# Performance work log

Hardware: AMD Instinct MI355X
Metric: run time of the kernel (lower is better)

Reference implementation:

```python
import jax, jax.numpy as jnp
import numpy as np

H = 256          # hidden_size
K = 3            # pointer hops
LAMDA = 3.0
EPS = 1e-8       # torch cosine_similarity eps
# dropout is treated as eval-mode (identity)


def _gru_cell(x, h, wi, wh, bi, bh):
    # torch GRUCell: gate order reset, update, new
    gx = x @ wi.T + bi            # (B, 3*4H)
    gh = h @ wh.T + bh
    xr, xz, xn = jnp.split(gx, 3, axis=-1)
    hr, hz, hn = jnp.split(gh, 3, axis=-1)
    r = jax.nn.sigmoid(xr + hr)
    z = jax.nn.sigmoid(xz + hz)
    n = jnp.tanh(xn + r * hn)
    return (1.0 - z) * n + z * h


def setup_inputs() -> dict:
    key = jax.random.key(0)
    ks = jax.random.split(key, 16)
    B, L = 128, 512
    d2, d4 = 2 * H, 4 * H
    sc = lambda i, shape, fan: jax.random.normal(ks[i], shape, jnp.float32) * (1.0 / np.sqrt(fan))
    return {
        "m": jax.random.normal(ks[0], (B, L, d2), jnp.float32),
        "s1": jax.random.normal(ks[1], (B, d4), jnp.float32),
        "s2": jax.random.normal(ks[2], (B, d4), jnp.float32),
        "s3": jax.random.normal(ks[3], (B, d4), jnp.float32),
        "m_mask": jnp.ones((B, L), jnp.int32),
        "w2_w": sc(4, (d2, d2), d2), "w2_b": jnp.zeros((d2,), jnp.float32),
        "w3_w": sc(5, (d4, d2), d4), "w3_b": jnp.zeros((d2,), jnp.float32),
        "w4_w": sc(6, (d4, d4), d4), "w4_b": jnp.zeros((d4,), jnp.float32),
        "w5_w": sc(7, (d4, 1), d4), "w5_b": jnp.zeros((1,), jnp.float32),
        "gru_wi": sc(8, (3 * d4, d2), d2),
        "gru_wh": sc(9, (3 * d4, d4), d4),
        "gru_bi": jnp.zeros((3 * d4,), jnp.float32),
        "gru_bh": jnp.zeros((3 * d4,), jnp.float32),
    }


def reference(m, s1, s2, s3, m_mask,
              w2_w, w2_b, w3_w, w3_b, w4_w, w4_b, w5_w, w5_b,
              gru_wi, gru_wh, gru_bi, gru_bh):
    # m: (B, L, 2H); s*: (B, 4H); m_mask: (B, L)
    mtt = m @ w2_w + w2_b                         # (B, L, 2H), loop-invariant
    m_norm = jnp.maximum(jnp.linalg.norm(mtt, axis=-1), EPS)  # (B, L)
    invalid = m_mask == 0

    def branch(st):
        for _ in range(K):
            stt = st @ w3_w + w3_b                # (B, 2H)
            s_norm = jnp.maximum(jnp.linalg.norm(stt, axis=-1), EPS)  # (B,)
            dot = jnp.einsum('bld,bd->bl', mtt, stt)
            att = LAMDA * dot / (m_norm * s_norm[:, None])
            att = jnp.where(invalid, -jnp.inf, att)
            p = jax.nn.softmax(att, axis=1)       # (B, L)
            f_att = jnp.einsum('bl,bld->bd', p, m)  # (B, 2H)
            st = _gru_cell(f_att, st, gru_wi, gru_wh, gru_bi, gru_bh)
        h = jax.nn.relu(st @ w4_w + w4_b)         # (B, 4H)
        return (h @ w5_w + w5_b)[:, 0]            # (B,)

    result = jnp.stack([branch(s1), branch(s2), branch(s3)], axis=1)  # (B, 3)
    return jax.nn.log_softmax(result, axis=1)
```

## Files before the change

kernel.cpp:

```cpp
#include <hip/hip_runtime.h>
#include <math.h>

constexpr int B  = 128;
constexpr int L  = 512;
constexpr int D2 = 512;
constexpr int D4 = 1024;
constexpr int G3 = 3072;
constexpr int R3 = 384;
constexpr int NC = 4096;
constexpr float LAMDA = 3.0f;
constexpr float EPSF  = 1e-8f;

typedef __attribute__((ext_vector_type(8))) short bf16x8;
typedef __attribute__((ext_vector_type(8))) short short8;
typedef __attribute__((ext_vector_type(4))) float f32x4;

__device__ __forceinline__ ushort f2bf(float v) {
  uint u = __builtin_bit_cast(uint, v);
  u = (u + 0x7fffu + ((u >> 16) & 1u)) >> 16;
  return (ushort)u;
}
__device__ __forceinline__ float bf2f(ushort h) {
  return __builtin_bit_cast(float, (uint)h << 16);
}
__device__ __forceinline__ float bflo(uint w) { return __builtin_bit_cast(float, w << 16); }
__device__ __forceinline__ float bfhi(uint w) { return __builtin_bit_cast(float, w & 0xffff0000u); }
__device__ __forceinline__ void split2(float v, ushort& h, ushort& l) {
  h = f2bf(v);
  l = f2bf(v - bf2f(h));
}
__device__ __forceinline__ void gload_lds16(const void* g, void* l) {
  __builtin_amdgcn_global_load_lds(
      (const __attribute__((address_space(1))) unsigned int*)g,
      (__attribute__((address_space(3))) unsigned int*)l, 16, 0, 0);
}

__global__ void k_init(const float* __restrict__ s1, const float* __restrict__ s2,
                       const float* __restrict__ s3, float* __restrict__ st3,
                       ushort* __restrict__ sth, ushort* __restrict__ stl,
                       float* __restrict__ snacc, float* __restrict__ cacc,
                       float* __restrict__ o3) {
  int idx = blockIdx.x * blockDim.x + threadIdx.x;
  if (idx < R3) { snacc[idx] = 0.f; cacc[idx] = 0.f; o3[idx] = 0.f; }
  int total = R3 * D4;
  for (; idx < total; idx += gridDim.x * blockDim.x) {
    int r = idx / D4, i = idx - r * D4;
    int k = r / B, b = r - k * B;
    const float* s = (k == 0) ? s1 : (k == 1) ? s2 : s3;
    float v = s[b * D4 + i];
    st3[idx] = v;
    if (sth) { ushort h, l; split2(v, h, l); sth[idx] = h; stl[idx] = l; }
  }
}

__global__ void k_conv_m(const float* __restrict__ m, ushort* __restrict__ mbf) {
  int idx = blockIdx.x * blockDim.x + threadIdx.x;
  const int total8 = (B * L * D2) / 8;
  for (; idx < total8; idx += gridDim.x * blockDim.x) {
    const float4* p = reinterpret_cast<const float4*>(m) + (size_t)idx * 2;
    float4 a = p[0], c = p[1];
    ushort o[8] = {f2bf(a.x), f2bf(a.y), f2bf(a.z), f2bf(a.w),
                   f2bf(c.x), f2bf(c.y), f2bf(c.z), f2bf(c.w)};
    *reinterpret_cast<uint4*>(mbf + (size_t)idx * 8) = *reinterpret_cast<const uint4*>(o);
  }
}

__global__ void k_w2t(const float* __restrict__ w2, ushort* __restrict__ w2t) {
  __shared__ ushort t[64][65];
  int bk = (blockIdx.x & 7) * 64, bn = (blockIdx.x >> 3) * 64;
  int tid = threadIdx.x;
#pragma unroll
  for (int i = 0; i < 16; ++i) {
    int e = tid + i * 256; int r = e >> 6, c = e & 63;
    t[r][c] = f2bf(w2[(bk + r) * 512 + bn + c]);
  }
  __syncthreads();
#pragma unroll
  for (int i = 0; i < 16; ++i) {
    int e = tid + i * 256; int r = e >> 6, c = e & 63;
    w2t[(bn + r) * 512 + bk + c] = t[c][r];
  }
}

__global__ void k_split_direct(const float* __restrict__ in, ushort* __restrict__ oh,
                               ushort* __restrict__ ol, int n4) {
  int idx = blockIdx.x * blockDim.x + threadIdx.x;
  for (; idx < n4; idx += gridDim.x * blockDim.x) {
    float4 v = reinterpret_cast<const float4*>(in)[idx];
    ushort4 h, l;
    split2(v.x, h.x, l.x); split2(v.y, h.y, l.y);
    split2(v.z, h.z, l.z); split2(v.w, h.w, l.w);
    reinterpret_cast<ushort4*>(oh)[idx] = h;
    reinterpret_cast<ushort4*>(ol)[idx] = l;
  }
}

__global__ void k_split_trans(const float* __restrict__ in, int K, int N,
                              ushort* __restrict__ oh, ushort* __restrict__ ol) {
  __shared__ float t[64][65];
  int bk = blockIdx.x * 64, bn = blockIdx.y * 64;
  int tid = threadIdx.x;
#pragma unroll
  for (int i = 0; i < 16; ++i) {
    int e = tid + i * 256; int r = e >> 6, c = e & 63;
    t[r][c] = in[(size_t)(bk + r) * N + bn + c];
  }
  __syncthreads();
#pragma unroll
  for (int i = 0; i < 16; ++i) {
    int e = tid + i * 256; int r = e >> 6, c = e & 63;
    ushort h, l;
    split2(t[c][r], h, l);
    oh[(size_t)(bn + r) * K + bk + c] = h;
    ol[(size_t)(bn + r) * K + bk + c] = l;
  }
}

__global__ void k_bcat2(const float* __restrict__ w3b, const float* __restrict__ gbh,
                        const float* __restrict__ w2w, float* __restrict__ bcat) {
  int idx = blockIdx.x * 256 + threadIdx.x;
  if (idx < D2) bcat[idx] = w3b[idx];
  else if (idx < D2 + G3) bcat[idx] = gbh[idx - D2];
  else if (idx < NC) {
    int e = idx - (D2 + G3);
    float s = 0.f;
    for (int d = 0; d < D2; ++d) s = fmaf(w3b[d], w2w[(size_t)e * D2 + d], s);
    bcat[idx] = s;
  }
}

__global__ __launch_bounds__(64) void k_gemm_wf(
    const ushort* __restrict__ Ahp, const ushort* __restrict__ Alp,
    const ushort* __restrict__ Bhp, const ushort* __restrict__ Blp,
    ushort* __restrict__ Ch, ushort* __restrict__ Cl) {
  const int ln = threadIdx.x;
  const int lrow = ln & 15, lk = ln >> 4;
  const int rowb = blockIdx.y * 64;
  const int colb = blockIdx.x * 64;
  size_t aoff[4], boff[4];
#pragma unroll
  for (int f = 0; f < 4; ++f) {
    aoff[f] = (size_t)(rowb + f * 16 + lrow) * D2 + lk * 8;
    boff[f] = (size_t)(colb + f * 16 + lrow) * D2 + lk * 8;
  }
  f32x4 acc[4][4] = {};
  for (int kc = 0; kc < D2; kc += 32) {
    bf16x8 ah[4], al[4], bh[4], bl[4];
#pragma unroll
    for (int f = 0; f < 4; ++f) {
      ah[f] = *reinterpret_cast<const bf16x8*>(Ahp + aoff[f] + kc);
      al[f] = *reinterpret_cast<const bf16x8*>(Alp + aoff[f] + kc);
      bh[f] = *reinterpret_cast<const bf16x8*>(Bhp + boff[f] + kc);
      bl[f] = *reinterpret_cast<const bf16x8*>(Blp + boff[f] + kc);
    }
#pragma unroll
    for (int rf = 0; rf < 4; ++rf)
#pragma unroll
      for (int cf = 0; cf < 4; ++cf) {
        acc[rf][cf] = __builtin_amdgcn_mfma_f32_16x16x32_bf16(ah[rf], bh[cf], acc[rf][cf], 0, 0, 0);
        acc[rf][cf] = __builtin_amdgcn_mfma_f32_16x16x32_bf16(al[rf], bh[cf], acc[rf][cf], 0, 0, 0);
        acc[rf][cf] = __builtin_amdgcn_mfma_f32_16x16x32_bf16(ah[rf], bl[cf], acc[rf][cf], 0, 0, 0);
      }
  }
#pragma unroll
  for (int rf = 0; rf < 4; ++rf)
#pragma unroll
    for (int cf = 0; cf < 4; ++cf) {
      int col = colb + cf * 16 + lrow;
#pragma unroll
      for (int j = 0; j < 4; ++j) {
        int row = rowb + rf * 16 + lk * 4 + j;
        ushort h, l;
        split2(acc[rf][cf][j], h, l);
        Ch[(size_t)row * D4 + col] = h;
        Cl[(size_t)row * D4 + col] = l;
      }
    }
}

__global__ __launch_bounds__(256, 2) void k_mnorm4(const ushort* __restrict__ mbf,
                                                   const ushort* __restrict__ w2t,
                                                   const float* __restrict__ b2,
                                                   float* __restrict__ norm2) {
  __shared__ ushort As[2][64 * 32];
  __shared__ ushort Bs[2][512 * 32];
  const int tid = threadIdx.x;
  const int wv = tid >> 6, ln = tid & 63;
  const int lrow = ln & 15, lk = ln >> 4;
  const size_t rowb = (size_t)blockIdx.x * 64;

  auto stage = [&](int buf, int kc) {
    {
      int li = wv * 64 + ln;
      int row = li >> 2, slot = li & 3;
      const ushort* src = mbf + (rowb + row) * 512 + kc + ((slot ^ (row & 3)) << 3);
      gload_lds16(src, &As[buf][(size_t)wv * 64 * 8]);
    }
#pragma unroll
    for (int i = 0; i < 8; ++i) {
      int c = wv * 8 + i;
      int li = c * 64 + ln;
      int col = li >> 2, slot = li & 3;
      const ushort* src = w2t + (size_t)col * 512 + kc + ((slot ^ (col & 3)) << 3);
      gload_lds16(src, &Bs[buf][(size_t)c * 64 * 8]);
    }
  };

  f32x4 acc[4][8] = {};
  stage(0, 0);
  __syncthreads();
  for (int t = 0; t < 16; ++t) {
    int cur = t & 1;
    if (t + 1 < 16) stage(cur ^ 1, (t + 1) * 32);
    bf16x8 af[4], bfr[8];
#pragma unroll
    for (int rf = 0; rf < 4; ++rf) {
      int row = rf * 16 + lrow;
      af[rf] = *reinterpret_cast<const bf16x8*>(&As[cur][row * 32 + ((lk ^ (row & 3)) << 3)]);
    }
#pragma unroll
    for (int cf = 0; cf < 8; ++cf) {
      int col = wv * 128 + cf * 16 + lrow;
      bfr[cf] = *reinterpret_cast<const bf16x8*>(&Bs[cur][col * 32 + ((lk ^ (col & 3)) << 3)]);
    }
#pragma unroll
    for (int rf = 0; rf < 4; ++rf)
#pragma unroll
      for (int cf = 0; cf < 8; ++cf)
        acc[rf][cf] = __builtin_amdgcn_mfma_f32_16x16x32_bf16(af[rf], bfr[cf], acc[rf][cf], 0, 0, 0);
    __syncthreads();
  }

  float nrm[4][4] = {};
#pragma unroll
  for (int cf = 0; cf < 8; ++cf) {
    float bb = b2[wv * 128 + cf * 16 + lrow];
#pragma unroll
    for (int rf = 0; rf < 4; ++rf)
#pragma unroll
      for (int j = 0; j < 4; ++j) {
        float v = acc[rf][cf][j] + bb;
        nrm[rf][j] = fmaf(v, v, nrm[rf][j]);
      }
  }
  __shared__ float red[4][64];
#pragma unroll
  for (int rf = 0; rf < 4; ++rf)
#pragma unroll
    for (int j = 0; j < 4; ++j) {
      float v = nrm[rf][j];
      v += __shfl_xor(v, 1); v += __shfl_xor(v, 2);
      v += __shfl_xor(v, 4); v += __shfl_xor(v, 8);
      if (lrow == 0) red[wv][rf * 16 + lk * 4 + j] = v;
    }
  __syncthreads();
  if (tid < 64)
    norm2[rowb + tid] = red[0][tid] + red[1][tid] + red[2][tid] + red[3][tid];
}

#define G3_LOAD(AH_, AL_, BH_, BL_, KC_)                                                    \
  do {                                                                                      \
    _Pragma("unroll") for (int f = 0; f < 2; ++f) {                                         \
      AH_[f] = *reinterpret_cast<const bf16x8*>(ah0 + (size_t)f * 16 * Kd + (KC_));         \
      AL_[f] = *reinterpret_cast<const bf16x8*>(al0 + (size_t)f * 16 * Kd + (KC_));         \
    }                                                                                       \
    _Pragma("unroll") for (int f = 0; f < 4; ++f) {                                         \
      BH_[f] = *reinterpret_cast<const bf16x8*>(bh0 + (size_t)f * 16 * Kd + (KC_));         \
      BL_[f] = *reinterpret_cast<const bf16x8*>(bl0 + (size_t)f * 16 * Kd + (KC_));         \
    }                                                                                       \
  } while (0)
#define G3_MFMA(AH_, AL_, BH_, BL_)                                                         \
  do {                                                                                      \
    _Pragma("unroll") for (int rf = 0; rf < 2; ++rf)                                        \
        _Pragma("unroll") for (int cf = 0; cf < 4; ++cf) {                                  \
      acc[rf][cf] = __builtin_amdgcn_mfma_f32_16x16x32_bf16(AH_[rf], BH_[cf], acc[rf][cf],  \
                                                            0, 0, 0);                       \
      acc[rf][cf] = __builtin_amdgcn_mfma_f32_16x16x32_bf16(AL_[rf], BH_[cf], acc[rf][cf],  \
                                                            0, 0, 0);                       \
      acc[rf][cf] = __builtin_amdgcn_mfma_f32_16x16x32_bf16(AH_[rf], BL_[cf], acc[rf][cf],  \
                                                            0, 0, 0);                       \
    }                                                                                       \
  } while (0)

template <int EPI>
__global__ __launch_bounds__(64) void k_gemm3(
    const ushort* __restrict__ Ahp, const ushort* __restrict__ Alp,
    const ushort* __restrict__ Bhp, const ushort* __restrict__ Blp,
    int Kd, const float* __restrict__ bias,
    float* __restrict__ outf, int ldc,
    float* __restrict__ gh, float* __restrict__ shat,
    float* __restrict__ snacc, float* __restrict__ cacc,
    const float* __restrict__ b2,
    const float* __restrict__ w5w, float* __restrict__ o3) {
  const int ln = threadIdx.x;
  const int lrow = ln & 15, lk = ln >> 4;
  const int rowb = blockIdx.y * 32;
  const int colb = blockIdx.x * 64;
  const ushort* ah0 = Ahp + (size_t)(rowb + lrow) * Kd + lk * 8;
  const ushort* al0 = Alp + (size_t)(rowb + lrow) * Kd + lk * 8;
  const ushort* bh0 = Bhp + (size_t)(colb + lrow) * Kd + lk * 8;
  const ushort* bl0 = Blp + (size_t)(colb + lrow) * Kd + lk * 8;
  f32x4 acc[2][4] = {};
  bf16x8 ahA[2], alA[2], bhA[4], blA[4];
  bf16x8 ahB[2], alB[2], bhB[4], blB[4];
  G3_LOAD(ahA, alA, bhA, blA, 0);
  for (int kc = 0; kc < Kd; kc += 64) {
    G3_LOAD(ahB, alB, bhB, blB, kc + 32);
    G3_MFMA(ahA, alA, bhA, blA);
    if (kc + 64 < Kd) G3_LOAD(ahA, alA, bhA, blA, kc + 64);
    G3_MFMA(ahB, alB, bhB, blB);
  }

  if (EPI == 0) {
#pragma unroll
    for (int rf = 0; rf < 2; ++rf)
#pragma unroll
      for (int cf = 0; cf < 4; ++cf) {
        int col = colb + cf * 16 + lrow;
        float bb = bias ? bias[col] : 0.f;
#pragma unroll
        for (int j = 0; j < 4; ++j) {
          int row = rowb + rf * 16 + lk * 4 + j;
          outf[(size_t)row * ldc + col] = acc[rf][cf][j] + bb;
        }
      }
  } else if (EPI == 1) {
    if (colb < D2) {
      float ss[2][4] = {}, sc[2][4] = {};
#pragma unroll
      for (int cf = 0; cf < 4; ++cf) {
        int col = colb + cf * 16 + lrow;
        float bb = bias[col], bc = b2[col];
#pragma unroll
        for (int rf = 0; rf < 2; ++rf)
#pragma unroll
          for (int j = 0; j < 4; ++j) {
            float v = acc[rf][cf][j] + bb;
            ss[rf][j] = fmaf(v, v, ss[rf][j]);
            sc[rf][j] = fmaf(v, bc, sc[rf][j]);
          }
      }
#pragma unroll
      for (int rf = 0; rf < 2; ++rf)
#pragma unroll
        for (int j = 0; j < 4; ++j) {
          float a = ss[rf][j], c = sc[rf][j];
          a += __shfl_xor(a, 1); c += __shfl_xor(c, 1);
          a += __shfl_xor(a, 2); c += __shfl_xor(c, 2);
          a += __shfl_xor(a, 4); c += __shfl_xor(c, 4);
          a += __shfl_xor(a, 8); c += __shfl_xor(c, 8);
          if (lrow == 0) {
            int row = rowb + rf * 16 + lk * 4 + j;
            atomicAdd(&snacc[row], a);
            atomicAdd(&cacc[row], c);
          }
        }
    } else {
#pragma unroll
      for (int rf = 0; rf < 2; ++rf)
#pragma unroll
        for (int cf = 0; cf < 4; ++cf) {
          int col = colb + cf * 16 + lrow;
          float bb = bias[col];
#pragma unroll
          for (int j = 0; j < 4; ++j) {
            int row = rowb + rf * 16 + lk * 4 + j;
            float v = acc[rf][cf][j] + bb;
            if (colb < D2 + G3) gh[(size_t)row * G3 + (col - D2)] = v;
            else                shat[(size_t)row * D2 + (col - (D2 + G3))] = v;
          }
        }
    }
  } else {
#pragma unroll
    for (int rf = 0; rf < 2; ++rf)
#pragma unroll
      for (int j = 0; j < 4; ++j) {
        float p = 0.f;
#pragma unroll
        for (int cf = 0; cf < 4; ++cf) {
          int col = colb + cf * 16 + lrow;
          float v = fmaxf(acc[rf][cf][j] + bias[col], 0.f);
          p = fmaf(v, w5w[col], p);
        }
        p += __shfl_xor(p, 1); p += __shfl_xor(p, 2);
        p += __shfl_xor(p, 4); p += __shfl_xor(p, 8);
        if (lrow == 0) atomicAdd(&o3[rowb + rf * 16 + lk * 4 + j], p);
      }
  }
}

__global__ __launch_bounds__(256) void k_dot_bf(const ushort* __restrict__ mbf,
                                                const float* __restrict__ shat3,
                                                const float* __restrict__ norm2,
                                                const float* __restrict__ snacc,
                                                const float* __restrict__ cacc,
                                                const int* __restrict__ mask,
                                                float* __restrict__ att3) {
  __shared__ float sh[3][512];
  int b = blockIdx.x >> 3;
  int lt = blockIdx.x & 7;
  int tid = threadIdx.x;
  for (int k = 0; k < 3; ++k)
    for (int i = tid; i < 512; i += 256) sh[k][i] = shat3[(size_t)(k * B + b) * D2 + i];
  __syncthreads();
  int j = tid & 3, lidx = tid >> 2;
  int l = lt * 64 + lidx;
  const uint4* mrow = reinterpret_cast<const uint4*>(mbf + (size_t)(b * L + l) * D2);
  float a0 = 0.f, a1 = 0.f, a2 = 0.f;
#pragma unroll 4
  for (int s = 0; s < 16; ++s) {
    int c = s * 4 + j;
    uint4 mv = mrow[c];
    const float* p0 = &sh[0][c * 8];
    const float* p1 = &sh[1][c * 8];
    const float* p2 = &sh[2][c * 8];
    uint w[4] = {mv.x, mv.y, mv.z, mv.w};
#pragma unroll
    for (int q = 0; q < 4; ++q) {
      float lo = bflo(w[q]), hi = bfhi(w[q]);
      a0 = fmaf(lo, p0[q * 2], a0); a0 = fmaf(hi, p0[q * 2 + 1], a0);
      a1 = fmaf(lo, p1[q * 2], a1); a1 = fmaf(hi, p1[q * 2 + 1], a1);
      a2 = fmaf(lo, p2[q * 2], a2); a2 = fmaf(hi, p2[q * 2 + 1], a2);
    }
  }
  a0 += __shfl_xor(a0, 1); a0 += __shfl_xor(a0, 2);
  a1 += __shfl_xor(a1, 1); a1 += __shfl_xor(a1, 2);
  a2 += __shfl_xor(a2, 1); a2 += __shfl_xor(a2, 2);
  if (j == 0) {
    float mn = fmaxf(sqrtf(norm2[b * L + l]), EPSF);
    bool inv = (mask[b * L + l] == 0);
    float ar[3] = {a0, a1, a2};
#pragma unroll
    for (int k = 0; k < 3; ++k) {
      int r = k * B + b;
      float sn = fmaxf(sqrtf(snacc[r]), EPSF);
      float att = LAMDA * (ar[k] + cacc[r]) / (mn * sn);
      att3[(size_t)r * L + l] = inv ? -INFINITY : att;
    }
  }
}

__global__ void k_softmax(float* __restrict__ att3) {
  int r = blockIdx.x;
  float* row = att3 + (size_t)r * L;
  int tid = threadIdx.x;
  float x0 = row[tid], x1 = row[tid + 256];
  float mx = fmaxf(x0, x1);
  for (int o = 32; o; o >>= 1) mx = fmaxf(mx, __shfl_xor(mx, o));
  __shared__ float rm[4], rs[4];
  int w = tid >> 6;
  if ((tid & 63) == 0) rm[w] = mx;
  __syncthreads();
  mx = fmaxf(fmaxf(rm[0], rm[1]), fmaxf(rm[2], rm[3]));
  float e0 = expf(x0 - mx), e1 = expf(x1 - mx);
  float s = e0 + e1;
  for (int o = 32; o; o >>= 1) s += __shfl_xor(s, o);
  if ((tid & 63) == 0) rs[w] = s;
  __syncthreads();
  s = rs[0] + rs[1] + rs[2] + rs[3];
  float inv = 1.0f / s;
  row[tid] = e0 * inv;
  row[tid + 256] = e1 * inv;
}

__global__ __launch_bounds__(256) void k_fatt_bf(const ushort* __restrict__ mbf,
                                                 const float* __restrict__ p3,
                                                 ushort* __restrict__ fatth,
                                                 ushort* __restrict__ fattl) {
  __shared__ float pp[3][512];
  __shared__ float red[3][256];
  int b = blockIdx.x >> 1, dt = blockIdx.x & 1;
  int tid = threadIdx.x;
  for (int k = 0; k < 3; ++k)
    for (int i = tid; i < 512; i += 256) pp[k][i] = p3[(size_t)(k * B + b) * L + i];
  __syncthreads();
  int dpair = tid & 127, half = tid >> 7;
  int d = dt * 256 + dpair * 2;
  float a[3][2] = {};
  int l0 = half * 256;
#pragma unroll 4
  for (int l = l0; l < l0 + 256; ++l) {
    uint w = *reinterpret_cast<const uint*>(&mbf[(size_t)(b * L + l) * D2 + d]);
    float f0 = bflo(w), f1 = bfhi(w);
#pragma unroll
    for (int k = 0; k < 3; ++k) {
      float p = pp[k][l];
      a[k][0] = fmaf(p, f0, a[k][0]);
      a[k][1] = fmaf(p, f1, a[k][1]);
    }
  }
  if (half == 1) {
#pragma unroll
    for (int k = 0; k < 3; ++k) { red[k][dpair * 2] = a[k][0]; red[k][dpair * 2 + 1] = a[k][1]; }
  }
  __syncthreads();
  if (half == 0) {
#pragma unroll
    for (int k = 0; k < 3; ++k) {
      float v0 = a[k][0] + red[k][dpair * 2];
      float v1 = a[k][1] + red[k][dpair * 2 + 1];
      ushort h0, l0u, h1, l1u;
      split2(v0, h0, l0u); split2(v1, h1, l1u);
      size_t o = (size_t)(k * B + b) * D2 + d;
      fatth[o] = h0;     fattl[o] = l0u;
      fatth[o + 1] = h1; fattl[o + 1] = l1u;
    }
  }
}

__global__ void k_gates(const float* __restrict__ gx, const float* __restrict__ gh,
                        float* __restrict__ st3,
                        ushort* __restrict__ sth, ushort* __restrict__ stl,
                        float* __restrict__ snacc, float* __restrict__ cacc) {
  int idx = blockIdx.x * blockDim.x + threadIdx.x;
  if (snacc && idx < R3) { snacc[idx] = 0.f; cacc[idx] = 0.f; }
  if (idx >= R3 * D4) return;
  int r = idx / D4, i = idx - r * D4;
  const float* gxr = gx + (size_t)r * G3;
  const float* ghr = gh + (size_t)r * G3;
  float xr = gxr[i], xz = gxr[D4 + i], xn = gxr[2 * D4 + i];
  float hr = ghr[i], hz = ghr[D4 + i], hn = ghr[2 * D4 + i];
  float rr = 1.f / (1.f + expf(-(xr + hr)));
  float zz = 1.f / (1.f + expf(-(xz + hz)));
  float nn = tanhf(xn + rr * hn);
  float h = st3[idx];
  float nv = (1.f - zz) * nn + zz * h;
  st3[idx] = nv;
  if (sth) { ushort hh, ll; split2(nv, hh, ll); sth[idx] = hh; stl[idx] = ll; }
}

__global__ void k_final(const float* __restrict__ o3, const float* __restrict__ w5b,
                        float* __restrict__ out) {
  int b = threadIdx.x;
  if (b >= B) return;
  float v0 = o3[0 * B + b] + w5b[0];
  float v1 = o3[1 * B + b] + w5b[0];
  float v2 = o3[2 * B + b] + w5b[0];
  float mx = fmaxf(v0, fmaxf(v1, v2));
  float s = expf(v0 - mx) + expf(v1 - mx) + expf(v2 - mx);
  float lse = mx + logf(s);
  out[b * 3 + 0] = v0 - lse;
  out[b * 3 + 1] = v1 - lse;
  out[b * 3 + 2] = v2 - lse;
}

__global__ __launch_bounds__(256) void k_mnorm(const float* __restrict__ m,
                                               const float* __restrict__ w2,
                                               const float* __restrict__ b2,
                                               float* __restrict__ norm2) {
  __shared__ float As[64][33];
  __shared__ float Ws[32][65];
  __shared__ float red[16][64];
  const int tid = threadIdx.x;
  const int ty = tid >> 4, tx = tid & 15;
  const long rowb = (long)blockIdx.x * 64;
  float rowpart[4] = {0.f, 0.f, 0.f, 0.f};
  for (int ct = 0; ct < 8; ++ct) {
    float acc[4][4] = {};
    for (int kc = 0; kc < 16; ++kc) {
#pragma unroll
      for (int i = 0; i < 8; ++i) {
        int li = tid + i * 256;
        int r = li >> 5, c = li & 31;
        As[r][c] = m[(rowb + r) * 512 + kc * 32 + c];
      }
#pragma unroll
      for (int i = 0; i < 8; ++i) {
        int li = tid + i * 256;
        int r = li >> 6, c = li & 63;
        Ws[r][c] = w2[(kc * 32 + r) * 512 + ct * 64 + c];
      }
      __syncthreads();
#pragma unroll
      for (int k = 0; k < 32; ++k) {
        float a[4], bb[4];
#pragma unroll
        for (int i = 0; i < 4; ++i) a[i] = As[ty * 4 + i][k];
#pragma unroll
        for (int jj = 0; jj < 4; ++jj) bb[jj] = Ws[k][tx * 4 + jj];
#pragma unroll
        for (int i = 0; i < 4; ++i)
#pragma unroll
          for (int jj = 0; jj < 4; ++jj) acc[i][jj] = fmaf(a[i], bb[jj], acc[i][jj]);
      }
      __syncthreads();
    }
#pragma unroll
    for (int jj = 0; jj < 4; ++jj) {
      float bj = b2[ct * 64 + tx * 4 + jj];
#pragma unroll
      for (int i = 0; i < 4; ++i) {
        float v = acc[i][jj] + bj;
        rowpart[i] = fmaf(v, v, rowpart[i]);
      }
    }
  }
#pragma unroll
  for (int i = 0; i < 4; ++i) red[tx][ty * 4 + i] = rowpart[i];
  __syncthreads();
  if (tid < 64) {
    float s = 0.f;
#pragma unroll
    for (int t = 0; t < 16; ++t) s += red[t][tid];
    norm2[rowb + tid] = s;
  }
}

template <bool BT, int ACT>
__global__ __launch_bounds__(256) void k_gemm64(const float* __restrict__ A, int lda,
                                                const float* __restrict__ Bm, int ldb,
                                                const float* __restrict__ bias,
                                                float* __restrict__ C, int ldc, int Kd) {
  __shared__ float As[64][33];
  __shared__ float Bs[32][65];
  const int tid = threadIdx.x;
  const int ty = tid >> 4, tx = tid & 15;
  const int rowb = blockIdx.y * 64;
  const int colb = blockIdx.x * 64;
  float acc[4][4] = {};
  for (int kc = 0; kc < Kd; kc += 32) {
#pragma unroll
    for (int i = 0; i < 8; ++i) {
      int li = tid + i * 256;
      int r = li >> 5, c = li & 31;
      As[r][c] = A[(long)(rowb + r) * lda + kc + c];
    }
    if (!BT) {
#pragma unroll
      for (int i = 0; i < 8; ++i) {
        int li = tid + i * 256;
        int r = li >> 6, c = li & 63;
        Bs[r][c] = Bm[(long)(kc + r) * ldb + colb + c];
      }
    } else {
#pragma unroll
      for (int i = 0; i < 8; ++i) {
        int li = tid + i * 256;
        int n = li >> 5, k = li & 31;
        Bs[k][n] = Bm[(long)(colb + n) * ldb + kc + k];
      }
    }
    __syncthreads();
#pragma unroll
    for (int k = 0; k < 32; ++k) {
      float a[4], bb[4];
#pragma unroll
      for (int i = 0; i < 4; ++i) a[i] = As[ty * 4 + i][k];
#pragma unroll
      for (int jj = 0; jj < 4; ++jj) bb[jj] = Bs[k][tx * 4 + jj];
#pragma unroll
      for (int i = 0; i < 4; ++i)
#pragma unroll
        for (int jj = 0; jj < 4; ++jj) acc[i][jj] = fmaf(a[i], bb[jj], acc[i][jj]);
    }
    __syncthreads();
  }
#pragma unroll
  for (int i = 0; i < 4; ++i) {
    int row = rowb + ty * 4 + i;
#pragma unroll
    for (int jj = 0; jj < 4; ++jj) {
      int col = colb + tx * 4 + jj;
      float v = acc[i][jj];
      if (bias) v += bias[col];
      if (ACT == 1) v = fmaxf(v, 0.f);
      C[(long)row * ldc + col] = v;
    }
  }
}

__global__ void k_snorm(const float* __restrict__ stt3, const float* __restrict__ b2,
                        float* __restrict__ sn3, float* __restrict__ c3) {
  int r = blockIdx.x;
  int tid = threadIdx.x;
  float ss = 0.f, sc = 0.f;
  for (int j = tid; j < D2; j += 256) {
    float v = stt3[(size_t)r * D2 + j];
    ss = fmaf(v, v, ss);
    sc = fmaf(v, b2[j], sc);
  }
  for (int o = 32; o; o >>= 1) {
    ss += __shfl_down(ss, o);
    sc += __shfl_down(sc, o);
  }
  __shared__ float rs[4], rc[4];
  int w = tid >> 6;
  if ((tid & 63) == 0) { rs[w] = ss; rc[w] = sc; }
  __syncthreads();
  if (tid == 0) {
    sn3[r] = fmaxf(sqrtf(rs[0] + rs[1] + rs[2] + rs[3]), EPSF);
    c3[r] = rc[0] + rc[1] + rc[2] + rc[3];
  }
}

__global__ __launch_bounds__(256) void k_dot(const float* __restrict__ m,
                                             const float* __restrict__ shat3,
                                             const float* __restrict__ norm2,
                                             const float* __restrict__ sn3,
                                             const float* __restrict__ c3,
                                             const int* __restrict__ mask,
                                             float* __restrict__ att3) {
  __shared__ float sh[3][512];
  int b = blockIdx.x >> 3;
  int lt = blockIdx.x & 7;
  int tid = threadIdx.x;
  for (int k = 0; k < 3; ++k)
    for (int i = tid; i < 512; i += 256) sh[k][i] = shat3[(size_t)(k * B + b) * D2 + i];
  __syncthreads();
  int j = tid & 3, lidx = tid >> 2;
  int l = lt * 64 + lidx;
  const float4* mrow = reinterpret_cast<const float4*>(m + (size_t)(b * L + l) * D2);
  float a0 = 0.f, a1 = 0.f, a2 = 0.f;
#pragma unroll 8
  for (int s = 0; s < 32; ++s) {
    int d4 = s * 4 + j;
    float4 mv = mrow[d4];
    const float4 v0 = *reinterpret_cast<const float4*>(&sh[0][d4 * 4]);
    const float4 v1 = *reinterpret_cast<const float4*>(&sh[1][d4 * 4]);
    const float4 v2 = *reinterpret_cast<const float4*>(&sh[2][d4 * 4]);
    a0 += mv.x * v0.x + mv.y * v0.y + mv.z * v0.z + mv.w * v0.w;
    a1 += mv.x * v1.x + mv.y * v1.y + mv.z * v1.z + mv.w * v1.w;
    a2 += mv.x * v2.x + mv.y * v2.y + mv.z * v2.z + mv.w * v2.w;
  }
  a0 += __shfl_xor(a0, 1); a0 += __shfl_xor(a0, 2);
  a1 += __shfl_xor(a1, 1); a1 += __shfl_xor(a1, 2);
  a2 += __shfl_xor(a2, 1); a2 += __shfl_xor(a2, 2);
  if (j == 0) {
    float mn = fmaxf(sqrtf(norm2[b * L + l]), EPSF);
    bool inv = (mask[b * L + l] == 0);
    float ar[3] = {a0, a1, a2};
#pragma unroll
    for (int k = 0; k < 3; ++k) {
      int r = k * B + b;
      float att = LAMDA * (ar[k] + c3[r]) / (mn * sn3[r]);
      att3[(size_t)r * L + l] = inv ? -INFINITY : att;
    }
  }
}

__global__ __launch_bounds__(256) void k_fatt(const float* __restrict__ m,
                                              const float* __restrict__ p3,
                                              float* __restrict__ fatt3) {
  __shared__ float pp[3][512];
  __shared__ float red[3][128];
  int b = blockIdx.x >> 2, dt = blockIdx.x & 3;
  int tid = threadIdx.x;
  for (int k = 0; k < 3; ++k)
    for (int i = tid; i < 512; i += 256) pp[k][i] = p3[(size_t)(k * B + b) * L + i];
  __syncthreads();
  int d = dt * 128 + (tid & 127);
  int half = tid >> 7;
  float a0 = 0.f, a1 = 0.f, a2 = 0.f;
  int l0 = half * 256;
  for (int l = l0; l < l0 + 256; ++l) {
    float mv = m[(size_t)(b * L + l) * D2 + d];
    a0 = fmaf(pp[0][l], mv, a0);
    a1 = fmaf(pp[1][l], mv, a1);
    a2 = fmaf(pp[2][l], mv, a2);
  }
  int dd = tid & 127;
  if (half == 1) { red[0][dd] = a0; red[1][dd] = a1; red[2][dd] = a2; }
  __syncthreads();
  if (half == 0) {
    fatt3[(size_t)(0 * B + b) * D2 + d] = a0 + red[0][dd];
    fatt3[(size_t)(1 * B + b) * D2 + d] = a1 + red[1][dd];
    fatt3[(size_t)(2 * B + b) * D2 + d] = a2 + red[2][dd];
  }
}

__global__ void k_w5(const float* __restrict__ h4, const float* __restrict__ w5w,
                     float* __restrict__ o3) {
  int r = blockIdx.x, tid = threadIdx.x;
  float s = 0.f;
  for (int d = tid; d < D4; d += 256) s = fmaf(h4[(size_t)r * D4 + d], w5w[d], s);
  for (int o = 32; o; o >>= 1) s += __shfl_down(s, o);
  __shared__ float rs[4];
  if ((tid & 63) == 0) rs[tid >> 6] = s;
  __syncthreads();
  if (tid == 0) o3[r] = rs[0] + rs[1] + rs[2] + rs[3];
}

extern "C" void kernel_launch(void* const* d_in, const int* in_sizes, int n_in,
                              void* d_out, int out_size, void* d_ws, size_t ws_size,
                              hipStream_t stream) {
  const float* m    = (const float*)d_in[0];
  const float* s1   = (const float*)d_in[1];
  const float* s2   = (const float*)d_in[2];
  const float* s3   = (const float*)d_in[3];
  const int*   mask = (const int*)d_in[4];
  const float* w2w  = (const float*)d_in[5];
  const float* w2b  = (const float*)d_in[6];
  const float* w3w  = (const float*)d_in[7];
  const float* w3b  = (const float*)d_in[8];
  const float* w4w  = (const float*)d_in[9];
  const float* w4b  = (const float*)d_in[10];
  const float* w5w  = (const float*)d_in[11];
  const float* w5b  = (const float*)d_in[12];
  const float* gwi  = (const float*)d_in[13];
  const float* gwh  = (const float*)d_in[14];
  const float* gbi  = (const float*)d_in[15];
  const float* gbh  = (const float*)d_in[16];
  float* out = (float*)d_out;

  float* ws = (float*)d_ws;
  size_t off = 0;
  auto alloc = [&](size_t n) {
    float* p = ws + off;
    off += (n + 63) & ~(size_t)63;
    return p;
  };
  ushort* mbf   = (ushort*)alloc((size_t)B * L * D2 / 2);
  ushort* w2t   = (ushort*)alloc((size_t)D2 * D2 / 2);
  ushort* catBh = (ushort*)alloc((size_t)NC * D4 / 2);
  ushort* catBl = (ushort*)alloc((size_t)NC * D4 / 2);
  ushort* gxBh  = (ushort*)alloc((size_t)G3 * D2 / 2);
  ushort* gxBl  = (ushort*)alloc((size_t)G3 * D2 / 2);
  ushort* w4Bh  = (ushort*)alloc((size_t)D4 * D4 / 2);
  ushort* w4Bl  = (ushort*)alloc((size_t)D4 * D4 / 2);
  float* bcat   = alloc(NC);
  float* norm2  = alloc((size_t)B * L);
  float* st3    = alloc((size_t)R3 * D4);
  ushort* sth   = (ushort*)alloc((size_t)R3 * D4 / 2);
  ushort* stl   = (ushort*)alloc((size_t)R3 * D4 / 2);
  float* shat3  = alloc((size_t)R3 * D2);
  float* snacc  = alloc(R3);
  float* cacc   = alloc(R3);
  float* o3     = alloc(R3);
  ushort* fatth = (ushort*)alloc((size_t)R3 * D2 / 2);
  ushort* fattl = (ushort*)alloc((size_t)R3 * D2 / 2);
  float* att3   = alloc((size_t)R3 * L);
  float* gx     = alloc((size_t)R3 * G3);
  float* gh     = alloc((size_t)R3 * G3);
  const size_t big_need = off;
  const bool big = ws_size >= big_need * sizeof(float);

  if (big) {
    ushort* w2dh = (ushort*)gh;
    ushort* w2dl = w2dh + (size_t)D2 * D2;
    ushort* w3dh = (ushort*)gx;
    ushort* w3dl = w3dh + (size_t)D4 * D2;

    k_init<<<1536, 256, 0, stream>>>(s1, s2, s3, st3, sth, stl, snacc, cacc, o3);
    k_conv_m<<<2048, 256, 0, stream>>>(m, mbf);
    k_w2t<<<64, 256, 0, stream>>>(w2w, w2t);
    k_mnorm4<<<(B * L) / 64, 256, 0, stream>>>(mbf, w2t, w2b, norm2);
    k_split_trans<<<dim3(D4 / 64, D2 / 64), 256, 0, stream>>>(w3w, D4, D2, catBh, catBl);
    k_split_direct<<<1024, 256, 0, stream>>>(gwh, catBh + (size_t)D2 * D4, catBl + (size_t)D2 * D4,
                                             (G3 * D4) / 4);
    k_split_direct<<<512, 256, 0, stream>>>(gwi, gxBh, gxBl, (G3 * D2) / 4);
    k_split_trans<<<dim3(D4 / 64, D4 / 64), 256, 0, stream>>>(w4w, D4, D4, w4Bh, w4Bl);
    k_split_direct<<<256, 256, 0, stream>>>(w2w, w2dh, w2dl, (D2 * D2) / 4);
    k_split_direct<<<256, 256, 0, stream>>>(w3w, w3dh, w3dl, (D4 * D2) / 4);
    k_bcat2<<<16, 256, 0, stream>>>(w3b, gbh, w2w, bcat);
    k_gemm_wf<<<dim3(D4 / 64, D2 / 64), 64, 0, stream>>>(
        w2dh, w2dl, w3dh, w3dl,
        catBh + (size_t)(D2 + G3) * D4, catBl + (size_t)(D2 + G3) * D4);

    for (int hop = 0; hop < 3; ++hop) {
      k_gemm3<1><<<dim3(NC / 64, R3 / 32), 64, 0, stream>>>(
          sth, stl, catBh, catBl, D4, bcat, nullptr, 0,
          gh, shat3, snacc, cacc, w2b, nullptr, nullptr);
      k_dot_bf<<<B * 8, 256, 0, stream>>>(mbf, shat3, norm2, snacc, cacc, mask, att3);
      k_softmax<<<3 * B, 256, 0, stream>>>(att3);
      k_fatt_bf<<<B * 2, 256, 0, stream>>>(mbf, att3, fatth, fattl);
      k_gemm3<0><<<dim3(G3 / 64, R3 / 32), 64, 0, stream>>>(
          fatth, fattl, gxBh, gxBl, D2, gbi, gx, G3,
          nullptr, nullptr, nullptr, nullptr, nullptr, nullptr, nullptr);
      k_gates<<<1536, 256, 0, stream>>>(gx, gh, st3, sth, stl, snacc, cacc);
    }
    k_gemm3<2><<<dim3(D4 / 64, R3 / 32), 64, 0, stream>>>(
        sth, stl, w4Bh, w4Bl, D4, w4b, nullptr, 0,
        nullptr, nullptr, nullptr, nullptr, nullptr, w5w, o3);
    k_final<<<1, 128, 0, stream>>>(o3, w5b, out);
  } else {
    off = 0;
    float* f_st3   = alloc((size_t)R3 * D4);
    float* f_norm2 = alloc((size_t)B * L);
    float* f_stt   = alloc((size_t)R3 * D2);
    float* f_shat  = alloc((size_t)R3 * D2);
    float* f_sn    = alloc(R3);
    float* f_c     = alloc(R3);
    float* f_att   = alloc((size_t)R3 * L);
    float* f_fatt  = alloc((size_t)R3 * D2);
    float* f_gx    = alloc((size_t)R3 * G3);
    float* f_gh    = alloc((size_t)R3 * G3);
    float* f_h4    = alloc((size_t)R3 * D4);
    float* f_o3    = alloc(R3);
    k_init<<<1536, 256, 0, stream>>>(s1, s2, s3, f_st3, nullptr, nullptr, f_sn, f_c, f_o3);
    k_mnorm<<<(B * L) / 64, 256, 0, stream>>>(m, w2w, w2b, f_norm2);
    for (int hop = 0; hop < 3; ++hop) {
      k_gemm64<false, 0><<<dim3(D2 / 64, R3 / 64), 256, 0, stream>>>(f_st3, D4, w3w, D2, w3b, f_stt, D2, D4);
      k_snorm<<<R3, 256, 0, stream>>>(f_stt, w2b, f_sn, f_c);
      k_gemm64<true, 0><<<dim3(D2 / 64, R3 / 64), 256, 0, stream>>>(f_stt, D2, w2w, D2, nullptr, f_shat, D2, D2);
      k_dot<<<B * 8, 256, 0, stream>>>(m, f_shat, f_norm2, f_sn, f_c, mask, f_att);
      k_softmax<<<3 * B, 256, 0, stream>>>(f_att);
      k_fatt<<<B * 4, 256, 0, stream>>>(m, f_att, f_fatt);
      k_gemm64<true, 0><<<dim3(G3 / 64, R3 / 64), 256, 0, stream>>>(f_fatt, D2, gwi, D2, gbi, f_gx, G3, D2);
      k_gemm64<true, 0><<<dim3(G3 / 64, R3 / 64), 256, 0, stream>>>(f_st3, D4, gwh, D4, gbh, f_gh, G3, D4);
      k_gates<<<1536, 256, 0, stream>>>(f_gx, f_gh, f_st3, nullptr, nullptr, nullptr, nullptr);
    }
    k_gemm64<false, 1><<<dim3(D4 / 64, R3 / 64), 256, 0, stream>>>(f_st3, D4, w4w, D4, w4b, f_h4, D4, D4);
    k_w5<<<R3, 256, 0, stream>>>(f_h4, w5w, f_o3);
    k_final<<<1, 128, 0, stream>>>(f_o3, w5b, out);
  }
}
```

Baseline: 479.3 us.

## Replace register-only split-bf16 GEMM with LDS-staged 64x256 tiled GEMM

The per-hop split-bf16 GEMM used one-wave blocks with 32x64 tiles that load operands straight from global memory into registers. It now uses 256-thread blocks with 64x256 tiles, staged through double-buffered, XOR-swizzled LDS via direct global-to-LDS loads, so A and B tiles are shared across the four waves. This cuts redundant global and L2 traffic but leaves far fewer blocks (e.g. 16x6 for the cat GEMM), which risks underfilling the GPU's CUs and adds barrier overhead on every k-step.

```diff
diff --git a/kernel.cpp b/kernel.cpp
--- a/kernel.cpp
+++ b/kernel.cpp
@@ -258,32 +258,8 @@
     norm2[rowb + tid] = red[0][tid] + red[1][tid] + red[2][tid] + red[3][tid];
 }
 
-#define G3_LOAD(AH_, AL_, BH_, BL_, KC_)                                                    \
-  do {                                                                                      \
-    _Pragma("unroll") for (int f = 0; f < 2; ++f) {                                         \
-      AH_[f] = *reinterpret_cast<const bf16x8*>(ah0 + (size_t)f * 16 * Kd + (KC_));         \
-      AL_[f] = *reinterpret_cast<const bf16x8*>(al0 + (size_t)f * 16 * Kd + (KC_));         \
-    }                                                                                       \
-    _Pragma("unroll") for (int f = 0; f < 4; ++f) {                                         \
-      BH_[f] = *reinterpret_cast<const bf16x8*>(bh0 + (size_t)f * 16 * Kd + (KC_));         \
-      BL_[f] = *reinterpret_cast<const bf16x8*>(bl0 + (size_t)f * 16 * Kd + (KC_));         \
-    }                                                                                       \
-  } while (0)
-#define G3_MFMA(AH_, AL_, BH_, BL_)                                                         \
-  do {                                                                                      \
-    _Pragma("unroll") for (int rf = 0; rf < 2; ++rf)                                        \
-        _Pragma("unroll") for (int cf = 0; cf < 4; ++cf) {                                  \
-      acc[rf][cf] = __builtin_amdgcn_mfma_f32_16x16x32_bf16(AH_[rf], BH_[cf], acc[rf][cf],  \
-                                                            0, 0, 0);                       \
-      acc[rf][cf] = __builtin_amdgcn_mfma_f32_16x16x32_bf16(AL_[rf], BH_[cf], acc[rf][cf],  \
-                                                            0, 0, 0);                       \
-      acc[rf][cf] = __builtin_amdgcn_mfma_f32_16x16x32_bf16(AH_[rf], BL_[cf], acc[rf][cf],  \
-                                                            0, 0, 0);                       \
-    }                                                                                       \
-  } while (0)
-
 template <int EPI>
-__global__ __launch_bounds__(64) void k_gemm3(
+__global__ __launch_bounds__(256) void k_gemm4(
     const ushort* __restrict__ Ahp, const ushort* __restrict__ Alp,
     const ushort* __restrict__ Bhp, const ushort* __restrict__ Blp,
     int Kd, const float* __restrict__ bias,
@@ -292,31 +268,74 @@
     float* __restrict__ snacc, float* __restrict__ cacc,
     const float* __restrict__ b2,
     const float* __restrict__ w5w, float* __restrict__ o3) {
-  const int ln = threadIdx.x;
+  __shared__ ushort AhS[2][64 * 32];
+  __shared__ ushort AlS[2][64 * 32];
+  __shared__ ushort BhS[2][256 * 32];
+  __shared__ ushort BlS[2][256 * 32];
+  const int tid = threadIdx.x;
+  const int wv = tid >> 6, ln = tid & 63;
   const int lrow = ln & 15, lk = ln >> 4;
-  const int rowb = blockIdx.y * 32;
-  const int colb = blockIdx.x * 64;
-  const ushort* ah0 = Ahp + (size_t)(rowb + lrow) * Kd + lk * 8;
-  const ushort* al0 = Alp + (size_t)(rowb + lrow) * Kd + lk * 8;
-  const ushort* bh0 = Bhp + (size_t)(colb + lrow) * Kd + lk * 8;
-  const ushort* bl0 = Blp + (size_t)(colb + lrow) * Kd + lk * 8;
-  f32x4 acc[2][4] = {};
-  bf16x8 ahA[2], alA[2], bhA[4], blA[4];
-  bf16x8 ahB[2], alB[2], bhB[4], blB[4];
-  G3_LOAD(ahA, alA, bhA, blA, 0);
-  for (int kc = 0; kc < Kd; kc += 64) {
-    G3_LOAD(ahB, alB, bhB, blB, kc + 32);
-    G3_MFMA(ahA, alA, bhA, blA);
-    if (kc + 64 < Kd) G3_LOAD(ahA, alA, bhA, blA, kc + 64);
-    G3_MFMA(ahB, alB, bhB, blB);
+  const int rowb = blockIdx.y * 64;
+  const int colb = blockIdx.x * 256;
+
+  auto stage = [&](int buf, int kc) {
+    {
+      int li = wv * 64 + ln;
+      int row = li >> 2, slot = li & 3;
+      int s = (slot ^ (row & 3)) << 3;
+      gload_lds16(Ahp + (size_t)(rowb + row) * Kd + kc + s, &AhS[buf][(size_t)wv * 64 * 8]);
+      gload_lds16(Alp + (size_t)(rowb + row) * Kd + kc + s, &AlS[buf][(size_t)wv * 64 * 8]);
+    }
+#pragma unroll
+    for (int i = 0; i < 4; ++i) {
+      int c = wv * 4 + i;
+      int li = c * 64 + ln;
+      int col = li >> 2, slot = li & 3;
+      int s = (slot ^ (col & 3)) << 3;
+      gload_lds16(Bhp + (size_t)(colb + col) * Kd + kc + s, &BhS[buf][(size_t)c * 64 * 8]);
+      gload_lds16(Blp + (size_t)(colb + col) * Kd + kc + s, &BlS[buf][(size_t)c * 64 * 8]);
+    }
+  };
+
+  f32x4 acc[4][4] = {};
+  const int nk = Kd >> 5;
+  stage(0, 0);
+  __syncthreads();
+  for (int t = 0; t < nk; ++t) {
+    int cur = t & 1;
+    if (t + 1 < nk) stage(cur ^ 1, (t + 1) * 32);
+    bf16x8 ah[4], al[4], bh[4], bl[4];
+#pragma unroll
+    for (int rf = 0; rf < 4; ++rf) {
+      int row = rf * 16 + lrow;
+      int off = row * 32 + ((lk ^ (row & 3)) << 3);
+      ah[rf] = *reinterpret_cast<const bf16x8*>(&AhS[cur][off]);
+      al[rf] = *reinterpret_cast<const bf16x8*>(&AlS[cur][off]);
+    }
+#pragma unroll
+    for (int cf = 0; cf < 4; ++cf) {
+      int col = wv * 64 + cf * 16 + lrow;
+      int off = col * 32 + ((lk ^ (col & 3)) << 3);
+      bh[cf] = *reinterpret_cast<const bf16x8*>(&BhS[cur][off]);
+      bl[cf] = *reinterpret_cast<const bf16x8*>(&BlS[cur][off]);
+    }
+#pragma unroll
+    for (int rf = 0; rf < 4; ++rf)
+#pragma unroll
+      for (int cf = 0; cf < 4; ++cf) {
+        acc[rf][cf] = __builtin_amdgcn_mfma_f32_16x16x32_bf16(ah[rf], bh[cf], acc[rf][cf], 0, 0, 0);
+        acc[rf][cf] = __builtin_amdgcn_mfma_f32_16x16x32_bf16(al[rf], bh[cf], acc[rf][cf], 0, 0, 0);
+        acc[rf][cf] = __builtin_amdgcn_mfma_f32_16x16x32_bf16(ah[rf], bl[cf], acc[rf][cf], 0, 0, 0);
+      }
+    __syncthreads();
   }
 
   if (EPI == 0) {
 #pragma unroll
-    for (int rf = 0; rf < 2; ++rf)
+    for (int rf = 0; rf < 4; ++rf)
 #pragma unroll
       for (int cf = 0; cf < 4; ++cf) {
-        int col = colb + cf * 16 + lrow;
+        int col = colb + wv * 64 + cf * 16 + lrow;
         float bb = bias ? bias[col] : 0.f;
 #pragma unroll
         for (int j = 0; j < 4; ++j) {
@@ -326,13 +345,13 @@
       }
   } else if (EPI == 1) {
     if (colb < D2) {
-      float ss[2][4] = {}, sc[2][4] = {};
+      float ss[4][4] = {}, sc[4][4] = {};
 #pragma unroll
       for (int cf = 0; cf < 4; ++cf) {
-        int col = colb + cf * 16 + lrow;
+        int col = colb + wv * 64 + cf * 16 + lrow;
         float bb = bias[col], bc = b2[col];
 #pragma unroll
-        for (int rf = 0; rf < 2; ++rf)
+        for (int rf = 0; rf < 4; ++rf)
 #pragma unroll
           for (int j = 0; j < 4; ++j) {
             float v = acc[rf][cf][j] + bb;
@@ -341,7 +360,7 @@
           }
       }
 #pragma unroll
-      for (int rf = 0; rf < 2; ++rf)
+      for (int rf = 0; rf < 4; ++rf)
 #pragma unroll
         for (int j = 0; j < 4; ++j) {
           float a = ss[rf][j], c = sc[rf][j];
@@ -357,29 +376,29 @@
         }
     } else {
 #pragma unroll
-      for (int rf = 0; rf < 2; ++rf)
+      for (int rf = 0; rf < 4; ++rf)
 #pragma unroll
         for (int cf = 0; cf < 4; ++cf) {
-          int col = colb + cf * 16 + lrow;
+          int col = colb + wv * 64 + cf * 16 + lrow;
           float bb = bias[col];
 #pragma unroll
           for (int j = 0; j < 4; ++j) {
             int row = rowb + rf * 16 + lk * 4 + j;
             float v = acc[rf][cf][j] + bb;
-            if (colb < D2 + G3) gh[(size_t)row * G3 + (col - D2)] = v;
-            else                shat[(size_t)row * D2 + (col - (D2 + G3))] = v;
+            if (col < D2 + G3) gh[(size_t)row * G3 + (col - D2)] = v;
+            else               shat[(size_t)row * D2 + (col - (D2 + G3))] = v;
           }
         }
     }
   } else {
 #pragma unroll
-    for (int rf = 0; rf < 2; ++rf)
+    for (int rf = 0; rf < 4; ++rf)
 #pragma unroll
       for (int j = 0; j < 4; ++j) {
         float p = 0.f;
 #pragma unroll
         for (int cf = 0; cf < 4; ++cf) {
-          int col = colb + cf * 16 + lrow;
+          int col = colb + wv * 64 + cf * 16 + lrow;
           float v = fmaxf(acc[rf][cf][j] + bias[col], 0.f);
           p = fmaf(v, w5w[col], p);
         }
@@ -858,18 +877,18 @@
         catBh + (size_t)(D2 + G3) * D4, catBl + (size_t)(D2 + G3) * D4);
 
     for (int hop = 0; hop < 3; ++hop) {
-      k_gemm3<1><<<dim3(NC / 64, R3 / 32), 64, 0, stream>>>(
+      k_gemm4<1><<<dim3(NC / 256, R3 / 64), 256, 0, stream>>>(
           sth, stl, catBh, catBl, D4, bcat, nullptr, 0,
           gh, shat3, snacc, cacc, w2b, nullptr, nullptr);
       k_dot_bf<<<B * 8, 256, 0, stream>>>(mbf, shat3, norm2, snacc, cacc, mask, att3);
       k_softmax<<<3 * B, 256, 0, stream>>>(att3);
       k_fatt_bf<<<B * 2, 256, 0, stream>>>(mbf, att3, fatth, fattl);
-      k_gemm3<0><<<dim3(G3 / 64, R3 / 32), 64, 0, stream>>>(
+      k_gemm4<0><<<dim3(G3 / 256, R3 / 64), 256, 0, stream>>>(
           fatth, fattl, gxBh, gxBl, D2, gbi, gx, G3,
           nullptr, nullptr, nullptr, nullptr, nullptr, nullptr, nullptr);
       k_gates<<<1536, 256, 0, stream>>>(gx, gh, st3, sth, stl, snacc, cacc);
     }
-    k_gemm3<2><<<dim3(D4 / 64, R3 / 32), 64, 0, stream>>>(
+    k_gemm4<2><<<dim3(D4 / 256, R3 / 64), 256, 0, stream>>>(
         sth, stl, w4Bh, w4Bl, D4, w4b, nullptr, 0,
         nullptr, nullptr, nullptr, nullptr, nullptr, w5w, o3);
     k_final<<<1, 128, 0, stream>>>(o3, w5b, out);
```

Result: slower. 538.8 us (+12.4%).

## Split K across four waves per block in GEMM kernel with LDS reduction

Applied to the files above, without the earlier changes.

The single-wave GEMM kernel becomes a 256-thread kernel where each of four waves processes a quarter of the K dimension. Partial accumulators from waves 1-3 are summed into wave 0 through shared memory before the existing epilogues. This is meant to cut per-block serial latency and raise occupancy for these small-M GEMMs. It adds an LDS round-trip and a barrier, and the epilogue then runs on only one wave.

```diff
diff --git a/kernel.cpp b/kernel.cpp
--- a/kernel.cpp
+++ b/kernel.cpp
@@ -283,7 +283,7 @@
   } while (0)
 
 template <int EPI>
-__global__ __launch_bounds__(64) void k_gemm3(
+__global__ __launch_bounds__(256) void k_gemm5(
     const ushort* __restrict__ Ahp, const ushort* __restrict__ Alp,
     const ushort* __restrict__ Bhp, const ushort* __restrict__ Blp,
     int Kd, const float* __restrict__ bias,
@@ -292,24 +292,49 @@
     float* __restrict__ snacc, float* __restrict__ cacc,
     const float* __restrict__ b2,
     const float* __restrict__ w5w, float* __restrict__ o3) {
-  const int ln = threadIdx.x;
+  __shared__ float red[3][32][64];
+  const int tid = threadIdx.x;
+  const int wv = tid >> 6, ln = tid & 63;
   const int lrow = ln & 15, lk = ln >> 4;
   const int rowb = blockIdx.y * 32;
   const int colb = blockIdx.x * 64;
-  const ushort* ah0 = Ahp + (size_t)(rowb + lrow) * Kd + lk * 8;
-  const ushort* al0 = Alp + (size_t)(rowb + lrow) * Kd + lk * 8;
-  const ushort* bh0 = Bhp + (size_t)(colb + lrow) * Kd + lk * 8;
-  const ushort* bl0 = Blp + (size_t)(colb + lrow) * Kd + lk * 8;
+  const int Ks = Kd >> 2;
+  const int koff = wv * Ks;
+  const ushort* ah0 = Ahp + (size_t)(rowb + lrow) * Kd + koff + lk * 8;
+  const ushort* al0 = Alp + (size_t)(rowb + lrow) * Kd + koff + lk * 8;
+  const ushort* bh0 = Bhp + (size_t)(colb + lrow) * Kd + koff + lk * 8;
+  const ushort* bl0 = Blp + (size_t)(colb + lrow) * Kd + koff + lk * 8;
   f32x4 acc[2][4] = {};
   bf16x8 ahA[2], alA[2], bhA[4], blA[4];
   bf16x8 ahB[2], alB[2], bhB[4], blB[4];
   G3_LOAD(ahA, alA, bhA, blA, 0);
-  for (int kc = 0; kc < Kd; kc += 64) {
+  for (int kc = 0; kc < Ks; kc += 64) {
     G3_LOAD(ahB, alB, bhB, blB, kc + 32);
     G3_MFMA(ahA, alA, bhA, blA);
-    if (kc + 64 < Kd) G3_LOAD(ahA, alA, bhA, blA, kc + 64);
+    if (kc + 64 < Ks) G3_LOAD(ahA, alA, bhA, blA, kc + 64);
     G3_MFMA(ahB, alB, bhB, blB);
   }
+
+  if (wv > 0) {
+#pragma unroll
+    for (int rf = 0; rf < 2; ++rf)
+#pragma unroll
+      for (int cf = 0; cf < 4; ++cf)
+#pragma unroll
+        for (int j = 0; j < 4; ++j)
+          red[wv - 1][(rf * 4 + cf) * 4 + j][ln] = acc[rf][cf][j];
+  }
+  __syncthreads();
+  if (wv != 0) return;
+#pragma unroll
+  for (int w = 0; w < 3; ++w)
+#pragma unroll
+    for (int rf = 0; rf < 2; ++rf)
+#pragma unroll
+      for (int cf = 0; cf < 4; ++cf)
+#pragma unroll
+        for (int j = 0; j < 4; ++j)
+          acc[rf][cf][j] += red[w][(rf * 4 + cf) * 4 + j][ln];
 
   if (EPI == 0) {
 #pragma unroll
@@ -858,18 +883,18 @@
         catBh + (size_t)(D2 + G3) * D4, catBl + (size_t)(D2 + G3) * D4);
 
     for (int hop = 0; hop < 3; ++hop) {
-      k_gemm3<1><<<dim3(NC / 64, R3 / 32), 64, 0, stream>>>(
+      k_gemm5<1><<<dim3(NC / 64, R3 / 32), 256, 0, stream>>>(
           sth, stl, catBh, catBl, D4, bcat, nullptr, 0,
           gh, shat3, snacc, cacc, w2b, nullptr, nullptr);
       k_dot_bf<<<B * 8, 256, 0, stream>>>(mbf, shat3, norm2, snacc, cacc, mask, att3);
       k_softmax<<<3 * B, 256, 0, stream>>>(att3);
       k_fatt_bf<<<B * 2, 256, 0, stream>>>(mbf, att3, fatth, fattl);
-      k_gemm3<0><<<dim3(G3 / 64, R3 / 32), 64, 0, stream>>>(
+      k_gemm5<0><<<dim3(G3 / 64, R3 / 32), 256, 0, stream>>>(
           fatth, fattl, gxBh, gxBl, D2, gbi, gx, G3,
           nullptr, nullptr, nullptr, nullptr, nullptr, nullptr, nullptr);
       k_gates<<<1536, 256, 0, stream>>>(gx, gh, st3, sth, stl, snacc, cacc);
     }
-    k_gemm3<2><<<dim3(D4 / 64, R3 / 32), 64, 0, stream>>>(
+    k_gemm5<2><<<dim3(D4 / 64, R3 / 32), 256, 0, stream>>>(
         sth, stl, w4Bh, w4Bl, D4, w4b, nullptr, 0,
         nullptr, nullptr, nullptr, nullptr, nullptr, w5w, o3);
     k_final<<<1, 128, 0, stream>>>(o3, w5b, out);
```

Result: no change. 477.6 us (-0.4%).
